# Performance work log

Hardware: AMD Instinct MI355X
Metric: run time of the kernel (lower is better)

Reference implementation:

```python
import jax, jax.numpy as jnp
import numpy as np

T, B, I, H, L = 256, 64, 512, 1024, 3


def _uniform(key, shape, stdv):
    return jax.random.uniform(key, shape, jnp.float32, -stdv, stdv)


def setup_inputs() -> dict:
    key = jax.random.key(0)
    ks = jax.random.split(key, 16)
    stdv = 1.0 / np.sqrt(H)
    inp = {
        "x": jax.random.normal(ks[0], (T, B, I), jnp.float32),
        "length": jax.random.randint(ks[1], (B,), 0, T).astype(jnp.int64),
        "h0": jnp.zeros((L, B, H), jnp.float32),
        "c0": jnp.zeros((L, B, H), jnp.float32),
        # layer 0: TopDownLSTMCell(input_size=I)
        "Wbh0": _uniform(ks[2], (I, 4 * H), stdv),
        "Whh0": _uniform(ks[3], (H, 4 * H), stdv),
        "Wth0": _uniform(ks[4], (H, 4 * H), stdv),
        "b0": jnp.zeros((4 * H,), jnp.float32),
        # layer 1: TopDownLSTMCell(input_size=H)
        "Wbh1": _uniform(ks[5], (H, 4 * H), stdv),
        "Whh1": _uniform(ks[6], (H, 4 * H), stdv),
        "Wth1": _uniform(ks[7], (H, 4 * H), stdv),
        "b1": jnp.zeros((4 * H,), jnp.float32),
        # layer 2: plain LSTMCell(input_size=H)
        "Wih2": _uniform(ks[8], (H, 4 * H), stdv),
        "Whh2": _uniform(ks[9], (H, 4 * H), stdv),
        "b2": jnp.zeros((4 * H,), jnp.float32),
    }
    return inp


def _gates(z, c0):
    # gate split order in source: f, i, o, g
    f, i, o, g = jnp.split(z, 4, axis=1)
    c1 = jax.nn.sigmoid(f) * c0 + jax.nn.sigmoid(i) * jnp.tanh(g)
    h1 = jax.nn.sigmoid(o) * jnp.tanh(c1)
    return h1, c1


def reference(x, length, h0, c0, Wbh0, Whh0, Wth0, b0,
              Wbh1, Whh1, Wth1, b1, Wih2, Whh2, b2):
    length = length.astype(jnp.int32)

    def step(carry, xs):
        Ht, C = carry              # [L, B, H]
        x_t, t = xs                # x_t: [B, I]
        m = (t < length)[:, None].astype(x_t.dtype)  # mask_time: freeze when t >= length

        # layer 0: bottom = x_t, top = Ht[1] (prev timestep, not yet updated)
        z = Ht[0] @ Whh0 + x_t @ Wbh0 + Ht[1] @ Wth0 + b0
        h1, c1 = _gates(z, C[0])
        Ht = Ht.at[0].set(m * h1 + (1 - m) * Ht[0])
        C = C.at[0].set(m * c1 + (1 - m) * C[0])

        # layer 1: bottom = Ht[0] (current step), top = Ht[2] (prev step); dropout=0 => identity
        z = Ht[1] @ Whh1 + Ht[0] @ Wbh1 + Ht[2] @ Wth1 + b1
        h1, c1 = _gates(z, C[1])
        Ht = Ht.at[1].set(m * h1 + (1 - m) * Ht[1])
        C = C.at[1].set(m * c1 + (1 - m) * C[1])

        # layer 2: plain LSTM cell on Ht[1] (current step)
        z = Ht[2] @ Whh2 + Ht[1] @ Wih2 + b2
        h1, c1 = _gates(z, C[2])
        h1 = m * h1 + (1 - m) * Ht[2]
        c1 = m * c1 + (1 - m) * C[2]
        Ht = Ht.at[2].set(h1)
        C = C.at[2].set(c1)
        return (Ht, C), h1

    (Ht, C), output = jax.lax.scan(step, (h0, c0), (x, jnp.arange(x.shape[0])))
    # batch_first=False -> output stays [T, B, H]
    return output, Ht, C
```

## Files before the change

### kernel.cpp

```cpp
#include <hip/hip_runtime.h>
#include <stdint.h>


using bf16x8 = __attribute__((ext_vector_type(8))) short;
using f32x4  = __attribute__((ext_vector_type(4))) float;

#define DEVINL __device__ __forceinline__

constexpr int T_ = 256;
constexpr int NBLK = 128;

constexpr size_t PIECE_ELEMS = 256ull * 1024 * 16;
constexpr size_t WP7_ELEMS   = 256ull * 512 * 16;
constexpr size_t WP_TOTAL    = 7 * PIECE_ELEMS + WP7_ELEMS;
constexpr size_t XB_OFF_B    = WP_TOTAL * 2;
constexpr size_t HB_OFF_B    = XB_OFF_B + 256ull * 64 * 512 * 2;
constexpr size_t HSLOT       = 3ull * 64 * 1024;
constexpr size_t SYNC_OFF_B  = HB_OFF_B + 3ull * HSLOT * 2;
constexpr size_t SYNC_BYTES  = 1024ull * 512;

DEVINL ushort f2bf(float f) {
  uint32_t x = __float_as_uint(f);
  uint32_t r = (x + 0x7fffu + ((x >> 16) & 1u)) >> 16;
  return (ushort)r;
}
DEVINL float sigf(float x) { return 1.0f / (1.0f + __expf(-x)); }
DEVINL float tanhf_(float x) {
  float ax = fabsf(x);
  float e  = __expf(-2.0f * ax);
  float t  = (1.0f - e) / (1.0f + e);
  return copysignf(t, x);
}

struct PackArgs { const float* src[8]; };

__global__ void pack_all(PackArgs pa, ushort* __restrict__ dst) {
  __shared__ ushort tile[1024 * 16];
  const int piece = blockIdx.y;
  const int K = (piece == 7) ? 512 : 1024;
  const float* __restrict__ src = pa.src[piece];
  const int b = blockIdx.x, tid = threadIdx.x;
  for (int idx = tid; idx < K * 4; idx += 256) {
    int k = idx >> 2, g = idx & 3;
    float4 v = *reinterpret_cast<const float4*>(src + (size_t)k * 4096 + g * 1024 + 4 * b);
    ushort* tp = &tile[k * 16 + g * 4];
    tp[0] = f2bf(v.x); tp[1] = f2bf(v.y); tp[2] = f2bf(v.z); tp[3] = f2bf(v.w);
  }
  __syncthreads();
  ushort* db = dst + (size_t)piece * PIECE_ELEMS + (size_t)b * K * 16;
  for (int o8 = tid; o8 < K * 2; o8 += 256) {
    int kb = o8 >> 4, c = o8 & 15;
    bf16x8 val;
#pragma unroll
    for (int i = 0; i < 8; ++i) val[i] = (short)tile[(kb * 8 + i) * 16 + c];
    *reinterpret_cast<bf16x8*>(db + (size_t)o8 * 8) = val;
  }
}

__global__ void cvt_x(const float* __restrict__ x, ushort* __restrict__ xb) {
  int i = blockIdx.x * blockDim.x + threadIdx.x;
  float4 v = reinterpret_cast<const float4*>(x)[i];
  ushort4 u;
  u.x = f2bf(v.x); u.y = f2bf(v.y); u.z = f2bf(v.z); u.w = f2bf(v.w);
  reinterpret_cast<ushort4*>(xb)[i] = u;
}

template <int K>
DEVINL void gemm2(f32x4 (&acc)[2][4], const ushort* __restrict__ A, int lda,
                  const ushort* __restrict__ Wb, int w, int r16, int q) {
  const int kw = (K / 8) * w;
  const ushort* wp = Wb + (size_t)q * 128 + (size_t)r16 * 8;
  const ushort* ap = A + r16 * lda + q * 8;
#pragma unroll
  for (int ks = 0; ks < K / 256; ++ks) {
    const int k0 = kw + ks * 32;
    const size_t wo = (size_t)(k0 >> 3) * 128;
    bf16x8 bf0 = __builtin_nontemporal_load(reinterpret_cast<const bf16x8*>(wp + wo));
    bf16x8 bf1 = __builtin_nontemporal_load(reinterpret_cast<const bf16x8*>(wp + wo + (size_t)K * 16));
    bf16x8 a0 = *reinterpret_cast<const bf16x8*>(ap + 0 * 16 * lda + k0);
    bf16x8 a1 = *reinterpret_cast<const bf16x8*>(ap + 1 * 16 * lda + k0);
    bf16x8 a2 = *reinterpret_cast<const bf16x8*>(ap + 2 * 16 * lda + k0);
    bf16x8 a3 = *reinterpret_cast<const bf16x8*>(ap + 3 * 16 * lda + k0);
    acc[0][0] = __builtin_amdgcn_mfma_f32_16x16x32_bf16(a0, bf0, acc[0][0], 0, 0, 0);
    acc[0][1] = __builtin_amdgcn_mfma_f32_16x16x32_bf16(a1, bf0, acc[0][1], 0, 0, 0);
    acc[0][2] = __builtin_amdgcn_mfma_f32_16x16x32_bf16(a2, bf0, acc[0][2], 0, 0, 0);
    acc[0][3] = __builtin_amdgcn_mfma_f32_16x16x32_bf16(a3, bf0, acc[0][3], 0, 0, 0);
    acc[1][0] = __builtin_amdgcn_mfma_f32_16x16x32_bf16(a0, bf1, acc[1][0], 0, 0, 0);
    acc[1][1] = __builtin_amdgcn_mfma_f32_16x16x32_bf16(a1, bf1, acc[1][1], 0, 0, 0);
    acc[1][2] = __builtin_amdgcn_mfma_f32_16x16x32_bf16(a2, bf1, acc[1][2], 0, 0, 0);
    acc[1][3] = __builtin_amdgcn_mfma_f32_16x16x32_bf16(a3, bf1, acc[1][3], 0, 0, 0);
  }
}

DEVINL void grid_barrier(int* __restrict__ syncp, int bar) {
  __builtin_amdgcn_fence(__ATOMIC_RELEASE, "agent");
  __syncthreads();
  int* base = syncp + (size_t)bar * 128;
  if (threadIdx.x == 0)
    __hip_atomic_fetch_add(base + (blockIdx.x & 7) * 16, 1,
                           __ATOMIC_RELAXED, __HIP_MEMORY_SCOPE_AGENT);
  if (threadIdx.x < 8) {
    while (__hip_atomic_load(base + threadIdx.x * 16,
                             __ATOMIC_RELAXED, __HIP_MEMORY_SCOPE_AGENT) < (NBLK / 8))
      __builtin_amdgcn_s_sleep(2);
  }
  __syncthreads();
  __builtin_amdgcn_fence(__ATOMIC_ACQUIRE, "agent");
}

__global__ void __launch_bounds__(512, 2)
lstm_persist(const ushort* __restrict__ Wp, const ushort* __restrict__ xb,
             ushort* __restrict__ Hb, int* __restrict__ syncp, float* __restrict__ outp,
             const float* __restrict__ h0, const float* __restrict__ c0,
             const int* __restrict__ len,
             const float* __restrict__ b0v, const float* __restrict__ b1v,
             const float* __restrict__ b2v) {
  const int pb = blockIdx.x, tid = threadIdx.x;
  const int w = tid >> 6, lane = tid & 63, r16 = lane & 15, q = lane >> 4;
  const int gr = tid >> 3, gj = tid & 7, g2g = gj >> 2, j4 = gj & 3;
  const int gcol = pb * 8 + g2g * 4 + j4;
  __shared__ float zp[8][2][64][17];

  int   mylen = len[gr];
  float h0r = h0[(0 * 64 + gr) * 1024 + gcol], c0r = c0[(0 * 64 + gr) * 1024 + gcol];
  float h1r = h0[(1 * 64 + gr) * 1024 + gcol], c1r = c0[(1 * 64 + gr) * 1024 + gcol];
  float h2r = h0[(2 * 64 + gr) * 1024 + gcol], c2r = c0[(2 * 64 + gr) * 1024 + gcol];
  float bb0[4], bb1[4], bb2[4];
#pragma unroll
  for (int g = 0; g < 4; ++g) {
    bb0[g] = b0v[g * 1024 + gcol];
    bb1[g] = b1v[g * 1024 + gcol];
    bb2[g] = b2v[g * 1024 + gcol];
  }

  {
    ushort* hs = Hb + 2 * HSLOT;
    hs[(0 * 64 + gr) * 1024 + gcol] = f2bf(h0r);
    hs[(1 * 64 + gr) * 1024 + gcol] = f2bf(h1r);
    hs[(2 * 64 + gr) * 1024 + gcol] = f2bf(h2r);
  }
  grid_barrier(syncp, 0);

  const ushort* Wp0 = Wp + 0 * PIECE_ELEMS;
  const ushort* Wp1 = Wp + 1 * PIECE_ELEMS;
  const ushort* Wp2 = Wp + 2 * PIECE_ELEMS;
  const ushort* Wp3 = Wp + 3 * PIECE_ELEMS;
  const ushort* Wp4 = Wp + 4 * PIECE_ELEMS;
  const ushort* Wp5 = Wp + 5 * PIECE_ELEMS;
  const ushort* Wp6 = Wp + 6 * PIECE_ELEMS;
  const ushort* Wp7 = Wp + 7 * PIECE_ELEMS;
  const size_t wb1024 = (size_t)(2 * pb) * 1024 * 16;
  const size_t wb512  = (size_t)(2 * pb) * 512 * 16;

  auto do_cell = [&](f32x4 (&acc)[2][4], const float* bb, float& hr, float& cr,
                     ushort* hbw, bool upd, float* ow) {
#pragma unroll
    for (int g2 = 0; g2 < 2; ++g2)
#pragma unroll
      for (int mf = 0; mf < 4; ++mf)
#pragma unroll
        for (int rg = 0; rg < 4; ++rg)
          zp[w][g2][mf * 16 + q * 4 + rg][r16] = acc[g2][mf][rg];
    __syncthreads();
    float z0 = bb[0], z1 = bb[1], z2 = bb[2], z3 = bb[3];
#pragma unroll
    for (int ww = 0; ww < 8; ++ww) {
      const float* zr = &zp[ww][g2g][gr][j4];
      z0 += zr[0]; z1 += zr[4]; z2 += zr[8]; z3 += zr[12];
    }
    float fg = sigf(z0), ig = sigf(z1), og = sigf(z2), gg = tanhf_(z3);
    float cn = fg * cr + ig * gg;
    float hn = og * tanhf_(cn);
    if (upd) { cr = cn; hr = hn; }
    hbw[gr * 1024 + gcol] = f2bf(hr);
    if (ow) ow[gr * 1024 + gcol] = hr;
    __syncthreads();
  };

  for (int t = 0; t < T_; ++t) {
    const int sC  = t % 3;
    const int sP  = (t + 2) % 3;
    const int sPP = (t + 1) % 3;
    ushort* HS_C        = Hb + (size_t)sC * HSLOT;
    const ushort* HS_P  = Hb + (size_t)sP * HSLOT;
    const ushort* HS_PP = Hb + (size_t)sPP * HSLOT;

    {
      f32x4 a0[2][4] = {{{0,0,0,0},{0,0,0,0},{0,0,0,0},{0,0,0,0}},
                        {{0,0,0,0},{0,0,0,0},{0,0,0,0},{0,0,0,0}}};
      f32x4 a2[2][4] = {{{0,0,0,0},{0,0,0,0},{0,0,0,0},{0,0,0,0}},
                        {{0,0,0,0},{0,0,0,0},{0,0,0,0},{0,0,0,0}}};
      gemm2<1024>(a0, HS_P + 0 * 65536, 1024, Wp0 + wb1024, w, r16, q);
      gemm2<1024>(a0, HS_P + 1 * 65536, 1024, Wp1 + wb1024, w, r16, q);
      gemm2<512 >(a0, xb + (size_t)t * 32768, 512, Wp7 + wb512, w, r16, q);
      if (t > 0) {
        gemm2<1024>(a2, HS_PP + 2 * 65536, 1024, Wp5 + wb1024, w, r16, q);
        gemm2<1024>(a2, HS_P  + 1 * 65536, 1024, Wp6 + wb1024, w, r16, q);
      }
      do_cell(a0, bb0, h0r, c0r, HS_C + 0 * 65536, t < mylen, nullptr);
      if (t > 0)
        do_cell(a2, bb2, h2r, c2r, Hb + (size_t)sP * HSLOT + 2 * 65536,
                (t - 1) < mylen, outp + (size_t)(t - 1) * 65536);
      grid_barrier(syncp, 1 + 2 * t);
    }
    {
      f32x4 a1[2][4] = {{{0,0,0,0},{0,0,0,0},{0,0,0,0},{0,0,0,0}},
                        {{0,0,0,0},{0,0,0,0},{0,0,0,0},{0,0,0,0}}};
      gemm2<1024>(a1, HS_P + 1 * 65536, 1024, Wp2 + wb1024, w, r16, q);
      gemm2<1024>(a1, HS_C + 0 * 65536, 1024, Wp3 + wb1024, w, r16, q);
      gemm2<1024>(a1, HS_P + 2 * 65536, 1024, Wp4 + wb1024, w, r16, q);
      do_cell(a1, bb1, h1r, c1r, HS_C + 1 * 65536, t < mylen, nullptr);
      grid_barrier(syncp, 2 + 2 * t);
    }
  }

  {
    const int t = T_;
    const int sP = (t + 2) % 3, sPP = (t + 1) % 3;
    f32x4 a2[2][4] = {{{0,0,0,0},{0,0,0,0},{0,0,0,0},{0,0,0,0}},
                      {{0,0,0,0},{0,0,0,0},{0,0,0,0},{0,0,0,0}}};
    gemm2<1024>(a2, Hb + (size_t)sPP * HSLOT + 2 * 65536, 1024, Wp5 + wb1024, w, r16, q);
    gemm2<1024>(a2, Hb + (size_t)sP  * HSLOT + 1 * 65536, 1024, Wp6 + wb1024, w, r16, q);
    do_cell(a2, bb2, h2r, c2r, Hb + (size_t)sP * HSLOT + 2 * 65536,
            (t - 1) < mylen, outp + (size_t)(t - 1) * 65536);
  }

  {
    float* HtO = outp + (size_t)T_ * 65536;
    float* CO  = HtO + 3 * 65536;
    HtO[(0 * 64 + gr) * 1024 + gcol] = h0r;
    HtO[(1 * 64 + gr) * 1024 + gcol] = h1r;
    HtO[(2 * 64 + gr) * 1024 + gcol] = h2r;
    CO[(0 * 64 + gr) * 1024 + gcol] = c0r;
    CO[(1 * 64 + gr) * 1024 + gcol] = c1r;
    CO[(2 * 64 + gr) * 1024 + gcol] = c2r;
  }
}

extern "C" void kernel_launch(void* const* d_in, const int* in_sizes, int n_in,
                              void* d_out, int out_size, void* d_ws, size_t ws_size,
                              hipStream_t stream) {
  (void)in_sizes; (void)n_in; (void)out_size; (void)ws_size;
  const float* x    = (const float*)d_in[0];
  const int*   len  = (const int*)d_in[1];
  const float* h0   = (const float*)d_in[2];
  const float* c0   = (const float*)d_in[3];
  const float* Wbh0 = (const float*)d_in[4];
  const float* Whh0 = (const float*)d_in[5];
  const float* Wth0 = (const float*)d_in[6];
  const float* b0   = (const float*)d_in[7];
  const float* Wbh1 = (const float*)d_in[8];
  const float* Whh1 = (const float*)d_in[9];
  const float* Wth1 = (const float*)d_in[10];
  const float* b1   = (const float*)d_in[11];
  const float* Wih2 = (const float*)d_in[12];
  const float* Whh2 = (const float*)d_in[13];
  const float* b2   = (const float*)d_in[14];

  ushort* Wp    = (ushort*)d_ws;
  ushort* xb    = (ushort*)((char*)d_ws + XB_OFF_B);
  ushort* Hb    = (ushort*)((char*)d_ws + HB_OFF_B);
  int*    syncp = (int*)((char*)d_ws + SYNC_OFF_B);

  PackArgs pa;
  pa.src[0] = Whh0; pa.src[1] = Wth0; pa.src[2] = Whh1; pa.src[3] = Wbh1;
  pa.src[4] = Wth1; pa.src[5] = Whh2; pa.src[6] = Wih2; pa.src[7] = Wbh0;
  pack_all<<<dim3(256, 8), 256, 0, stream>>>(pa, Wp);
  cvt_x<<<8192, 256, 0, stream>>>(x, xb);
  (void)hipMemsetAsync(syncp, 0, SYNC_BYTES, stream);

  lstm_persist<<<NBLK, 512, 0, stream>>>(Wp, xb, Hb, syncp, (float*)d_out,
                                         h0, c0, len, b0, b1, b2);
}
```

Baseline: 24.07 ms.

## Keep bf16 weights register-resident in a 256-block persistent LSTM kernel

```diff
diff --git a/kernel.cpp b/kernel.cpp
--- a/kernel.cpp
+++ b/kernel.cpp
@@ -8,16 +8,13 @@
 #define DEVINL __device__ __forceinline__
 
 constexpr int T_ = 256;
-constexpr int NBLK = 128;
-
-constexpr size_t PIECE_ELEMS = 256ull * 1024 * 16;
-constexpr size_t WP7_ELEMS   = 256ull * 512 * 16;
-constexpr size_t WP_TOTAL    = 7 * PIECE_ELEMS + WP7_ELEMS;
-constexpr size_t XB_OFF_B    = WP_TOTAL * 2;
-constexpr size_t HB_OFF_B    = XB_OFF_B + 256ull * 64 * 512 * 2;
-constexpr size_t HSLOT       = 3ull * 64 * 1024;
-constexpr size_t SYNC_OFF_B  = HB_OFF_B + 3ull * HSLOT * 2;
-constexpr size_t SYNC_BYTES  = 1024ull * 512;
+constexpr int NBLK = 256;
+
+constexpr size_t XB_ELEMS   = 256ull * 64 * 512;
+constexpr size_t HB_OFF_B   = XB_ELEMS * 2;
+constexpr size_t HSLOT      = 3ull * 64 * 1024;
+constexpr size_t SYNC_OFF_B = HB_OFF_B + 3ull * HSLOT * 2;
+constexpr size_t SYNC_BYTES = 520ull * 128 * 4;
 
 DEVINL ushort f2bf(float f) {
   uint32_t x = __float_as_uint(f);
@@ -32,31 +29,6 @@
   return copysignf(t, x);
 }
 
-struct PackArgs { const float* src[8]; };
-
-__global__ void pack_all(PackArgs pa, ushort* __restrict__ dst) {
-  __shared__ ushort tile[1024 * 16];
-  const int piece = blockIdx.y;
-  const int K = (piece == 7) ? 512 : 1024;
-  const float* __restrict__ src = pa.src[piece];
-  const int b = blockIdx.x, tid = threadIdx.x;
-  for (int idx = tid; idx < K * 4; idx += 256) {
-    int k = idx >> 2, g = idx & 3;
-    float4 v = *reinterpret_cast<const float4*>(src + (size_t)k * 4096 + g * 1024 + 4 * b);
-    ushort* tp = &tile[k * 16 + g * 4];
-    tp[0] = f2bf(v.x); tp[1] = f2bf(v.y); tp[2] = f2bf(v.z); tp[3] = f2bf(v.w);
-  }
-  __syncthreads();
-  ushort* db = dst + (size_t)piece * PIECE_ELEMS + (size_t)b * K * 16;
-  for (int o8 = tid; o8 < K * 2; o8 += 256) {
-    int kb = o8 >> 4, c = o8 & 15;
-    bf16x8 val;
-#pragma unroll
-    for (int i = 0; i < 8; ++i) val[i] = (short)tile[(kb * 8 + i) * 16 + c];
-    *reinterpret_cast<bf16x8*>(db + (size_t)o8 * 8) = val;
-  }
-}
-
 __global__ void cvt_x(const float* __restrict__ x, ushort* __restrict__ xb) {
   int i = blockIdx.x * blockDim.x + threadIdx.x;
   float4 v = reinterpret_cast<const float4*>(x)[i];
@@ -65,30 +37,21 @@
   reinterpret_cast<ushort4*>(xb)[i] = u;
 }
 
-template <int K>
-DEVINL void gemm2(f32x4 (&acc)[2][4], const ushort* __restrict__ A, int lda,
-                  const ushort* __restrict__ Wb, int w, int r16, int q) {
-  const int kw = (K / 8) * w;
-  const ushort* wp = Wb + (size_t)q * 128 + (size_t)r16 * 8;
-  const ushort* ap = A + r16 * lda + q * 8;
-#pragma unroll
-  for (int ks = 0; ks < K / 256; ++ks) {
-    const int k0 = kw + ks * 32;
-    const size_t wo = (size_t)(k0 >> 3) * 128;
-    bf16x8 bf0 = __builtin_nontemporal_load(reinterpret_cast<const bf16x8*>(wp + wo));
-    bf16x8 bf1 = __builtin_nontemporal_load(reinterpret_cast<const bf16x8*>(wp + wo + (size_t)K * 16));
-    bf16x8 a0 = *reinterpret_cast<const bf16x8*>(ap + 0 * 16 * lda + k0);
-    bf16x8 a1 = *reinterpret_cast<const bf16x8*>(ap + 1 * 16 * lda + k0);
-    bf16x8 a2 = *reinterpret_cast<const bf16x8*>(ap + 2 * 16 * lda + k0);
-    bf16x8 a3 = *reinterpret_cast<const bf16x8*>(ap + 3 * 16 * lda + k0);
-    acc[0][0] = __builtin_amdgcn_mfma_f32_16x16x32_bf16(a0, bf0, acc[0][0], 0, 0, 0);
-    acc[0][1] = __builtin_amdgcn_mfma_f32_16x16x32_bf16(a1, bf0, acc[0][1], 0, 0, 0);
-    acc[0][2] = __builtin_amdgcn_mfma_f32_16x16x32_bf16(a2, bf0, acc[0][2], 0, 0, 0);
-    acc[0][3] = __builtin_amdgcn_mfma_f32_16x16x32_bf16(a3, bf0, acc[0][3], 0, 0, 0);
-    acc[1][0] = __builtin_amdgcn_mfma_f32_16x16x32_bf16(a0, bf1, acc[1][0], 0, 0, 0);
-    acc[1][1] = __builtin_amdgcn_mfma_f32_16x16x32_bf16(a1, bf1, acc[1][1], 0, 0, 0);
-    acc[1][2] = __builtin_amdgcn_mfma_f32_16x16x32_bf16(a2, bf1, acc[1][2], 0, 0, 0);
-    acc[1][3] = __builtin_amdgcn_mfma_f32_16x16x32_bf16(a3, bf1, acc[1][3], 0, 0, 0);
+template <int NKS, int BASE>
+DEVINL void gemm_r(f32x4 (&acc)[4], const bf16x8 (&wf)[30],
+                   const ushort* __restrict__ A, int lda, int w, int r16, int q) {
+#pragma unroll
+  for (int ks = 0; ks < NKS; ++ks) {
+    const int k0 = NKS * 32 * w + 32 * ks;
+    const ushort* ap = A + r16 * lda + k0 + q * 8;
+    bf16x8 a0 = *reinterpret_cast<const bf16x8*>(ap);
+    bf16x8 a1 = *reinterpret_cast<const bf16x8*>(ap + 16 * lda);
+    bf16x8 a2 = *reinterpret_cast<const bf16x8*>(ap + 32 * lda);
+    bf16x8 a3 = *reinterpret_cast<const bf16x8*>(ap + 48 * lda);
+    acc[0] = __builtin_amdgcn_mfma_f32_16x16x32_bf16(a0, wf[BASE + ks], acc[0], 0, 0, 0);
+    acc[1] = __builtin_amdgcn_mfma_f32_16x16x32_bf16(a1, wf[BASE + ks], acc[1], 0, 0, 0);
+    acc[2] = __builtin_amdgcn_mfma_f32_16x16x32_bf16(a2, wf[BASE + ks], acc[2], 0, 0, 0);
+    acc[3] = __builtin_amdgcn_mfma_f32_16x16x32_bf16(a3, wf[BASE + ks], acc[3], 0, 0, 0);
   }
 }
 
@@ -102,38 +65,65 @@
   if (threadIdx.x < 8) {
     while (__hip_atomic_load(base + threadIdx.x * 16,
                              __ATOMIC_RELAXED, __HIP_MEMORY_SCOPE_AGENT) < (NBLK / 8))
-      __builtin_amdgcn_s_sleep(2);
+      __builtin_amdgcn_s_sleep(1);
   }
   __syncthreads();
   __builtin_amdgcn_fence(__ATOMIC_ACQUIRE, "agent");
 }
 
 __global__ void __launch_bounds__(512, 2)
-lstm_persist(const ushort* __restrict__ Wp, const ushort* __restrict__ xb,
-             ushort* __restrict__ Hb, int* __restrict__ syncp, float* __restrict__ outp,
+lstm_persist(const ushort* __restrict__ xb, ushort* __restrict__ Hb,
+             int* __restrict__ syncp, float* __restrict__ outp,
              const float* __restrict__ h0, const float* __restrict__ c0,
              const int* __restrict__ len,
+             const float* __restrict__ Whh0, const float* __restrict__ Wth0,
+             const float* __restrict__ Whh1, const float* __restrict__ Wbh1,
+             const float* __restrict__ Wth1, const float* __restrict__ Whh2,
+             const float* __restrict__ Wih2, const float* __restrict__ Wbh0,
              const float* __restrict__ b0v, const float* __restrict__ b1v,
              const float* __restrict__ b2v) {
   const int pb = blockIdx.x, tid = threadIdx.x;
   const int w = tid >> 6, lane = tid & 63, r16 = lane & 15, q = lane >> 4;
-  const int gr = tid >> 3, gj = tid & 7, g2g = gj >> 2, j4 = gj & 3;
-  const int gcol = pb * 8 + g2g * 4 + j4;
-  __shared__ float zp[8][2][64][17];
-
-  int   mylen = len[gr];
-  float h0r = h0[(0 * 64 + gr) * 1024 + gcol], c0r = c0[(0 * 64 + gr) * 1024 + gcol];
-  float h1r = h0[(1 * 64 + gr) * 1024 + gcol], c1r = c0[(1 * 64 + gr) * 1024 + gcol];
-  float h2r = h0[(2 * 64 + gr) * 1024 + gcol], c2r = c0[(2 * 64 + gr) * 1024 + gcol];
-  float bb0[4], bb1[4], bb2[4];
-#pragma unroll
-  for (int g = 0; g < 4; ++g) {
-    bb0[g] = b0v[g * 1024 + gcol];
-    bb1[g] = b1v[g * 1024 + gcol];
-    bb2[g] = b2v[g * 1024 + gcol];
-  }
-
-  {
+  __shared__ float zp[8][64][17];
+
+  const float* wsrc[8] = {Whh0, Wth0, Whh1, Wbh1, Wth1, Whh2, Wih2, Wbh0};
+  const int colW = (r16 >> 2) * 1024 + 4 * pb + (r16 & 3);
+  bf16x8 wf[30];
+#pragma unroll
+  for (int p = 0; p < 7; ++p)
+#pragma unroll
+    for (int ks = 0; ks < 4; ++ks) {
+      bf16x8 v;
+#pragma unroll
+      for (int i = 0; i < 8; ++i)
+        v[i] = (short)f2bf(wsrc[p][(size_t)(128 * w + 32 * ks + 8 * q + i) * 4096 + colW]);
+      wf[p * 4 + ks] = v;
+    }
+#pragma unroll
+  for (int ks = 0; ks < 2; ++ks) {
+    bf16x8 v;
+#pragma unroll
+    for (int i = 0; i < 8; ++i)
+      v[i] = (short)f2bf(wsrc[7][(size_t)(64 * w + 32 * ks + 8 * q + i) * 4096 + colW]);
+    wf[28 + ks] = v;
+  }
+
+  const int gr = tid >> 2, gj = tid & 3;
+  const int gcol = 4 * pb + gj;
+  int   mylen = 0;
+  float h0r = 0, h1r = 0, h2r = 0, c0r = 0, c1r = 0, c2r = 0;
+  float bb0[4] = {0,0,0,0}, bb1[4] = {0,0,0,0}, bb2[4] = {0,0,0,0};
+  if (tid < 256) {
+    mylen = len[gr];
+    h0r = h0[(0 * 64 + gr) * 1024 + gcol]; c0r = c0[(0 * 64 + gr) * 1024 + gcol];
+    h1r = h0[(1 * 64 + gr) * 1024 + gcol]; c1r = c0[(1 * 64 + gr) * 1024 + gcol];
+    h2r = h0[(2 * 64 + gr) * 1024 + gcol]; c2r = c0[(2 * 64 + gr) * 1024 + gcol];
+#pragma unroll
+    for (int g = 0; g < 4; ++g) {
+      bb0[g] = b0v[g * 1024 + gcol];
+      bb1[g] = b1v[g * 1024 + gcol];
+      bb2[g] = b2v[g * 1024 + gcol];
+    }
     ushort* hs = Hb + 2 * HSLOT;
     hs[(0 * 64 + gr) * 1024 + gcol] = f2bf(h0r);
     hs[(1 * 64 + gr) * 1024 + gcol] = f2bf(h1r);
@@ -141,39 +131,28 @@
   }
   grid_barrier(syncp, 0);
 
-  const ushort* Wp0 = Wp + 0 * PIECE_ELEMS;
-  const ushort* Wp1 = Wp + 1 * PIECE_ELEMS;
-  const ushort* Wp2 = Wp + 2 * PIECE_ELEMS;
-  const ushort* Wp3 = Wp + 3 * PIECE_ELEMS;
-  const ushort* Wp4 = Wp + 4 * PIECE_ELEMS;
-  const ushort* Wp5 = Wp + 5 * PIECE_ELEMS;
-  const ushort* Wp6 = Wp + 6 * PIECE_ELEMS;
-  const ushort* Wp7 = Wp + 7 * PIECE_ELEMS;
-  const size_t wb1024 = (size_t)(2 * pb) * 1024 * 16;
-  const size_t wb512  = (size_t)(2 * pb) * 512 * 16;
-
-  auto do_cell = [&](f32x4 (&acc)[2][4], const float* bb, float& hr, float& cr,
+  auto do_cell = [&](f32x4 (&acc)[4], const float* bb, float& hr, float& cr,
                      ushort* hbw, bool upd, float* ow) {
 #pragma unroll
-    for (int g2 = 0; g2 < 2; ++g2)
-#pragma unroll
-      for (int mf = 0; mf < 4; ++mf)
-#pragma unroll
-        for (int rg = 0; rg < 4; ++rg)
-          zp[w][g2][mf * 16 + q * 4 + rg][r16] = acc[g2][mf][rg];
+    for (int mf = 0; mf < 4; ++mf)
+#pragma unroll
+      for (int rg = 0; rg < 4; ++rg)
+        zp[w][mf * 16 + q * 4 + rg][r16] = acc[mf][rg];
     __syncthreads();
-    float z0 = bb[0], z1 = bb[1], z2 = bb[2], z3 = bb[3];
-#pragma unroll
-    for (int ww = 0; ww < 8; ++ww) {
-      const float* zr = &zp[ww][g2g][gr][j4];
-      z0 += zr[0]; z1 += zr[4]; z2 += zr[8]; z3 += zr[12];
-    }
-    float fg = sigf(z0), ig = sigf(z1), og = sigf(z2), gg = tanhf_(z3);
-    float cn = fg * cr + ig * gg;
-    float hn = og * tanhf_(cn);
-    if (upd) { cr = cn; hr = hn; }
-    hbw[gr * 1024 + gcol] = f2bf(hr);
-    if (ow) ow[gr * 1024 + gcol] = hr;
+    if (tid < 256) {
+      float z0 = bb[0], z1 = bb[1], z2 = bb[2], z3 = bb[3];
+#pragma unroll
+      for (int ww = 0; ww < 8; ++ww) {
+        const float* zr = &zp[ww][gr][0];
+        z0 += zr[gj]; z1 += zr[4 + gj]; z2 += zr[8 + gj]; z3 += zr[12 + gj];
+      }
+      float fg = sigf(z0), ig = sigf(z1), og = sigf(z2), gg = tanhf_(z3);
+      float cn = fg * cr + ig * gg;
+      float hn = og * tanhf_(cn);
+      if (upd) { cr = cn; hr = hn; }
+      hbw[gr * 1024 + gcol] = f2bf(hr);
+      if (ow) ow[gr * 1024 + gcol] = hr;
+    }
     __syncthreads();
   };
 
@@ -186,46 +165,41 @@
     const ushort* HS_PP = Hb + (size_t)sPP * HSLOT;
 
     {
-      f32x4 a0[2][4] = {{{0,0,0,0},{0,0,0,0},{0,0,0,0},{0,0,0,0}},
-                        {{0,0,0,0},{0,0,0,0},{0,0,0,0},{0,0,0,0}}};
-      f32x4 a2[2][4] = {{{0,0,0,0},{0,0,0,0},{0,0,0,0},{0,0,0,0}},
-                        {{0,0,0,0},{0,0,0,0},{0,0,0,0},{0,0,0,0}}};
-      gemm2<1024>(a0, HS_P + 0 * 65536, 1024, Wp0 + wb1024, w, r16, q);
-      gemm2<1024>(a0, HS_P + 1 * 65536, 1024, Wp1 + wb1024, w, r16, q);
-      gemm2<512 >(a0, xb + (size_t)t * 32768, 512, Wp7 + wb512, w, r16, q);
+      f32x4 aA[4] = {{0,0,0,0},{0,0,0,0},{0,0,0,0},{0,0,0,0}};
+      f32x4 aC[4] = {{0,0,0,0},{0,0,0,0},{0,0,0,0},{0,0,0,0}};
+      gemm_r<4, 0 >(aA, wf, HS_P + 0 * 65536, 1024, w, r16, q);
+      gemm_r<4, 4 >(aA, wf, HS_P + 1 * 65536, 1024, w, r16, q);
+      gemm_r<2, 28>(aA, wf, xb + (size_t)t * 32768, 512, w, r16, q);
       if (t > 0) {
-        gemm2<1024>(a2, HS_PP + 2 * 65536, 1024, Wp5 + wb1024, w, r16, q);
-        gemm2<1024>(a2, HS_P  + 1 * 65536, 1024, Wp6 + wb1024, w, r16, q);
+        gemm_r<4, 20>(aC, wf, HS_PP + 2 * 65536, 1024, w, r16, q);
+        gemm_r<4, 24>(aC, wf, HS_P  + 1 * 65536, 1024, w, r16, q);
       }
-      do_cell(a0, bb0, h0r, c0r, HS_C + 0 * 65536, t < mylen, nullptr);
+      do_cell(aA, bb0, h0r, c0r, HS_C + 0 * 65536, t < mylen, nullptr);
       if (t > 0)
-        do_cell(a2, bb2, h2r, c2r, Hb + (size_t)sP * HSLOT + 2 * 65536,
+        do_cell(aC, bb2, h2r, c2r, Hb + (size_t)sP * HSLOT + 2 * 65536,
                 (t - 1) < mylen, outp + (size_t)(t - 1) * 65536);
       grid_barrier(syncp, 1 + 2 * t);
     }
     {
-      f32x4 a1[2][4] = {{{0,0,0,0},{0,0,0,0},{0,0,0,0},{0,0,0,0}},
-                        {{0,0,0,0},{0,0,0,0},{0,0,0,0},{0,0,0,0}}};
-      gemm2<1024>(a1, HS_P + 1 * 65536, 1024, Wp2 + wb1024, w, r16, q);
-      gemm2<1024>(a1, HS_C + 0 * 65536, 1024, Wp3 + wb1024, w, r16, q);
-      gemm2<1024>(a1, HS_P + 2 * 65536, 1024, Wp4 + wb1024, w, r16, q);
-      do_cell(a1, bb1, h1r, c1r, HS_C + 1 * 65536, t < mylen, nullptr);
+      f32x4 aB[4] = {{0,0,0,0},{0,0,0,0},{0,0,0,0},{0,0,0,0}};
+      gemm_r<4, 8 >(aB, wf, HS_P + 1 * 65536, 1024, w, r16, q);
+      gemm_r<4, 12>(aB, wf, HS_C + 0 * 65536, 1024, w, r16, q);
+      gemm_r<4, 16>(aB, wf, HS_P + 2 * 65536, 1024, w, r16, q);
+      do_cell(aB, bb1, h1r, c1r, HS_C + 1 * 65536, t < mylen, nullptr);
       grid_barrier(syncp, 2 + 2 * t);
     }
   }
 
   {
-    const int t = T_;
-    const int sP = (t + 2) % 3, sPP = (t + 1) % 3;
-    f32x4 a2[2][4] = {{{0,0,0,0},{0,0,0,0},{0,0,0,0},{0,0,0,0}},
-                      {{0,0,0,0},{0,0,0,0},{0,0,0,0},{0,0,0,0}}};
-    gemm2<1024>(a2, Hb + (size_t)sPP * HSLOT + 2 * 65536, 1024, Wp5 + wb1024, w, r16, q);
-    gemm2<1024>(a2, Hb + (size_t)sP  * HSLOT + 1 * 65536, 1024, Wp6 + wb1024, w, r16, q);
-    do_cell(a2, bb2, h2r, c2r, Hb + (size_t)sP * HSLOT + 2 * 65536,
-            (t - 1) < mylen, outp + (size_t)(t - 1) * 65536);
-  }
-
-  {
+    const int sP = (T_ + 2) % 3, sPP = (T_ + 1) % 3;
+    f32x4 aC[4] = {{0,0,0,0},{0,0,0,0},{0,0,0,0},{0,0,0,0}};
+    gemm_r<4, 20>(aC, wf, Hb + (size_t)sPP * HSLOT + 2 * 65536, 1024, w, r16, q);
+    gemm_r<4, 24>(aC, wf, Hb + (size_t)sP  * HSLOT + 1 * 65536, 1024, w, r16, q);
+    do_cell(aC, bb2, h2r, c2r, Hb + (size_t)sP * HSLOT + 2 * 65536,
+            (T_ - 1) < mylen, outp + (size_t)(T_ - 1) * 65536);
+  }
+
+  if (tid < 256) {
     float* HtO = outp + (size_t)T_ * 65536;
     float* CO  = HtO + 3 * 65536;
     HtO[(0 * 64 + gr) * 1024 + gcol] = h0r;
@@ -257,18 +231,15 @@
   const float* Whh2 = (const float*)d_in[13];
   const float* b2   = (const float*)d_in[14];
 
-  ushort* Wp    = (ushort*)d_ws;
-  ushort* xb    = (ushort*)((char*)d_ws + XB_OFF_B);
+  ushort* xb    = (ushort*)d_ws;
   ushort* Hb    = (ushort*)((char*)d_ws + HB_OFF_B);
   int*    syncp = (int*)((char*)d_ws + SYNC_OFF_B);
 
-  PackArgs pa;
-  pa.src[0] = Whh0; pa.src[1] = Wth0; pa.src[2] = Whh1; pa.src[3] = Wbh1;
-  pa.src[4] = Wth1; pa.src[5] = Whh2; pa.src[6] = Wih2; pa.src[7] = Wbh0;
-  pack_all<<<dim3(256, 8), 256, 0, stream>>>(pa, Wp);
   cvt_x<<<8192, 256, 0, stream>>>(x, xb);
   (void)hipMemsetAsync(syncp, 0, SYNC_BYTES, stream);
 
-  lstm_persist<<<NBLK, 512, 0, stream>>>(Wp, xb, Hb, syncp, (float*)d_out,
-                                         h0, c0, len, b0, b1, b2);
-}
+  lstm_persist<<<NBLK, 512, 0, stream>>>(xb, Hb, syncp, (float*)d_out,
+                                         h0, c0, len,
+                                         Whh0, Wth0, Whh1, Wbh1, Wth1, Whh2,
+                                         Wih2, Wbh0, b0, b1, b2);
+}
```

Measured after the change: 30.11 ms. +25.1%, slower.
